# Optimization experiments

Measured on AMD Instinct MI355X. Metric: run time of the kernel, lower is better.

Reference implementation:

```python
import jax, jax.numpy as jnp
import numpy as np

NUM_SUBSET = 3
BN_EPS = 1e-5


def setup_inputs() -> dict:
    key = jax.random.key(0)
    ks = jax.random.split(key, 6)
    N, C, T, V = 32, 192, 256, 25
    x = jax.random.normal(ks[0], (N, C, T, V), dtype=jnp.float32)
    w_in = jax.random.normal(ks[1], (3 * C, C), dtype=jnp.float32) * (1.0 / np.sqrt(C))
    b_in = jax.random.normal(ks[2], (3 * C,), dtype=jnp.float32) * 0.02
    w_ff = jax.random.normal(ks[3], (C, C), dtype=jnp.float32) * (1.0 / np.sqrt(C))
    b_ff = jax.random.normal(ks[4], (C,), dtype=jnp.float32) * 0.02
    bn_gamma = jnp.ones((C,), dtype=jnp.float32)
    bn_beta = jnp.zeros((C,), dtype=jnp.float32)
    bn_mean = jnp.zeros((C,), dtype=jnp.float32)
    bn_var = jnp.ones((C,), dtype=jnp.float32)
    return dict(x=x, w_in=w_in, b_in=b_in, w_ff=w_ff, b_ff=b_ff,
                bn_gamma=bn_gamma, bn_beta=bn_beta, bn_mean=bn_mean, bn_var=bn_var)


def reference(x, w_in, b_in, w_ff, b_ff, bn_gamma, bn_beta, bn_mean, bn_var):
    N, C, T, V = x.shape
    S = NUM_SUBSET
    mid = C // S
    # 1x1 conv QKV projection: (N,C,T,V) x (3C,C) -> (N,3C,T,V)
    qkv = jnp.einsum('nctv,dc->ndtv', x, w_in) + b_in[None, :, None, None]
    qkv = qkv.reshape(N, 3 * S, mid, T, V)
    q, k, v = jnp.split(qkv, 3, axis=1)  # each (N,S,mid,T,V)
    # tanh-normalized attention over time: (N,S,T,T)
    att = jnp.tanh(jnp.einsum('nsctv,nscqv->nstq', q, k) / (mid * V))
    y = jnp.einsum('nstq,nscqv->nsctv', att, v).reshape(N, C, T, V)
    # ff_nett: 1x1 conv + BatchNorm (inference form)
    y = jnp.einsum('nctv,dc->ndtv', y, w_ff) + b_ff[None, :, None, None]
    inv = bn_gamma / jnp.sqrt(bn_var + BN_EPS)
    y = (y - bn_mean[None, :, None, None]) * inv[None, :, None, None] + bn_beta[None, :, None, None]
    # residual + LeakyReLU(0.1)
    z = x + y
    return jnp.where(z >= 0, z, 0.1 * z)
```

## Files before the change

### kernel.cpp

```cpp
#include <hip/hip_runtime.h>

#define TV 6400
#define NCH 192
#define D3 576

typedef unsigned short u16;
typedef unsigned int   u32;

typedef __attribute__((ext_vector_type(8))) short bf16x8;
typedef __attribute__((ext_vector_type(4))) float f32x4;

__device__ __forceinline__ float bf2f(u32 h) { return __uint_as_float(h << 16); }
__device__ __forceinline__ u16 f2bf(float f) {
    u32 u = __float_as_uint(f);
    return (u16)((u + 0x7FFFu + ((u >> 16) & 1u)) >> 16);
}

__global__ __launch_bounds__(256) void k_wcast(const float* __restrict__ w_in,
                                               const float* __restrict__ w_ff,
                                               u32* __restrict__ wb) {
    int i = blockIdx.x * 256 + threadIdx.x;
    float2 f;
    if (i < 55296) f = *(const float2*)(w_in + 2 * i);
    else           f = *(const float2*)(w_ff + 2 * (i - 55296));
    wb[i] = (u32)f2bf(f.x) | ((u32)f2bf(f.y) << 16);
}

__global__ __launch_bounds__(256) void k_trx(const float* __restrict__ x,
                                             u16* __restrict__ x_t) {
    const int p0 = blockIdx.x * 128, c0 = blockIdx.y * 64, n = blockIdx.z;
    const int tid = threadIdx.x;
    __shared__ float L[64][129];
    const float* xn = x + ((size_t)n * NCH + c0) * TV + p0;
#pragma unroll
    for (int r = 0; r < 8; ++r) {
        int idx = tid + 256 * r;
        int c = idx >> 5, p4 = idx & 31;
        float4 v = *(const float4*)(xn + (size_t)c * TV + p4 * 4);
        *(float4*)&L[c][p4 * 4] = v;
    }
    __syncthreads();
    const int row = tid >> 1, ch = (tid & 1) * 32;
    u16* dst = x_t + ((size_t)n * TV + p0 + row) * 192 + c0 + ch;
    u32 buf[16];
#pragma unroll
    for (int j = 0; j < 16; ++j) {
        float f0 = L[ch + 2 * j][row], f1 = L[ch + 2 * j + 1][row];
        buf[j] = (u32)f2bf(f0) | ((u32)f2bf(f1) << 16);
    }
#pragma unroll
    for (int q = 0; q < 4; ++q) {
        uint4 u; u.x = buf[q * 4]; u.y = buf[q * 4 + 1]; u.z = buf[q * 4 + 2]; u.w = buf[q * 4 + 3];
        *(uint4*)(dst + q * 8) = u;
    }
}

__global__ __launch_bounds__(256) void k_qkv(const u16* __restrict__ x_t,
                                             const u16* __restrict__ w_inb,
                                             const float* __restrict__ b_in,
                                             u16* __restrict__ qkv,
                                             u16* __restrict__ qt,
                                             u16* __restrict__ kt) {
    const int p0 = blockIdx.x * 128, n = blockIdx.y;
    const int tid = threadIdx.x;
    const int wid = tid >> 6, lane = tid & 63;
    const int wm = wid & 1, wn = wid >> 1;
    const int ml = lane & 15, kq = lane >> 4;

    __shared__ __align__(16) char Bs[128 * 384];
    __shared__ __align__(16) char As[64 * 384];

#pragma unroll
    for (int r = 0; r < 12; ++r) {
        int idx = tid + 256 * r;
        int row = idx / 24, g = idx - row * 24;
        uint4 v = *(const uint4*)(x_t + ((size_t)n * TV + p0 + row) * 192 + g * 8);
        *(uint4*)(Bs + row * 384 + (((g & ~7) | ((g ^ row) & 7)) << 4)) = v;
    }

    for (int dt = 0; dt < 9; ++dt) {
#pragma unroll
        for (int r = 0; r < 6; ++r) {
            int idx = tid + 256 * r;
            int row = idx / 24, g = idx - row * 24;
            uint4 v = *(const uint4*)(w_inb + (size_t)(dt * 64 + row) * 192 + g * 8);
            *(uint4*)(As + row * 384 + (((g & ~7) | ((g ^ row) & 7)) << 4)) = v;
        }
        __syncthreads();

        f32x4 acc[2][4];
#pragma unroll
        for (int i = 0; i < 2; i++)
#pragma unroll
            for (int j = 0; j < 4; j++)
#pragma unroll
                for (int r = 0; r < 4; r++) acc[i][j][r] = 0.f;

#pragma unroll
        for (int kk = 0; kk < 3; ++kk)
#pragma unroll
            for (int ks = 0; ks < 2; ++ks) {
                int g = kk * 8 + ks * 4 + kq;
                bf16x8 aw[2], bx[4];
#pragma unroll
                for (int mt = 0; mt < 2; ++mt) {
                    int row = wm * 32 + mt * 16 + ml;
                    aw[mt] = *(const bf16x8*)(As + row * 384 + (((g & ~7) | ((g ^ row) & 7)) << 4));
                }
#pragma unroll
                for (int nt = 0; nt < 4; ++nt) {
                    int row = wn * 64 + nt * 16 + ml;
                    bx[nt] = *(const bf16x8*)(Bs + row * 384 + (((g & ~7) | ((g ^ row) & 7)) << 4));
                }
#pragma unroll
                for (int mt = 0; mt < 2; ++mt)
#pragma unroll
                    for (int nt = 0; nt < 4; ++nt)
                        acc[mt][nt] = __builtin_amdgcn_mfma_f32_16x16x32_bf16(aw[mt], bx[nt], acc[mt][nt], 0, 0, 0);
            }

        if (dt < 6) {
            const int s = (dt < 3) ? dt : dt - 3;
            u16* dstb = (dt < 3 ? qt : kt) + ((size_t)(n * 3 + s) * 6400 + p0) * 64;
#pragma unroll
            for (int mt = 0; mt < 2; ++mt) {
                int c = wm * 32 + mt * 16 + kq * 4;
                float4 bias = *(const float4*)(b_in + dt * 64 + c);
#pragma unroll
                for (int nt = 0; nt < 4; ++nt) {
                    int p = wn * 64 + nt * 16 + ml;
                    u32 w0 = (u32)f2bf(acc[mt][nt][0] + bias.x) | ((u32)f2bf(acc[mt][nt][1] + bias.y) << 16);
                    u32 w1 = (u32)f2bf(acc[mt][nt][2] + bias.z) | ((u32)f2bf(acc[mt][nt][3] + bias.w) << 16);
                    uint2 u; u.x = w0; u.y = w1;
                    *(uint2*)(dstb + (size_t)p * 64 + c) = u;
                }
            }
        } else {
#pragma unroll
            for (int mt = 0; mt < 2; ++mt) {
                int d = dt * 64 + wm * 32 + mt * 16 + kq * 4;
                float4 bias = *(const float4*)(b_in + d);
                u16* vdst = qkv + ((size_t)n * D3 + d) * TV;
#pragma unroll
                for (int nt = 0; nt < 4; ++nt) {
                    int p = p0 + wn * 64 + nt * 16 + ml;
                    vdst[(size_t)0 * TV + p] = f2bf(acc[mt][nt][0] + bias.x);
                    vdst[(size_t)1 * TV + p] = f2bf(acc[mt][nt][1] + bias.y);
                    vdst[(size_t)2 * TV + p] = f2bf(acc[mt][nt][2] + bias.z);
                    vdst[(size_t)3 * TV + p] = f2bf(acc[mt][nt][3] + bias.w);
                }
            }
        }
        __syncthreads();
    }
}

__global__ __launch_bounds__(256) void k_scores(const u16* __restrict__ qt,
                                                const u16* __restrict__ kt,
                                                u16* __restrict__ att) {
    const int b = blockIdx.z, t0 = blockIdx.y * 128, q0 = blockIdx.x * 64;
    const int tid = threadIdx.x;
    const int wid = tid >> 6, lane = tid & 63;
    const int wm = wid & 1, wn = wid >> 1;
    const int ml = lane & 15, kq = lane >> 4;

    __shared__ __align__(16) char As[128 * 128];
    __shared__ __align__(16) char Bs[64 * 128];

    f32x4 acc[4][2];
#pragma unroll
    for (int i = 0; i < 4; i++)
#pragma unroll
        for (int j = 0; j < 2; j++)
#pragma unroll
            for (int r = 0; r < 4; r++) acc[i][j][r] = 0.f;

    const u16* qb = qt + (size_t)b * 256 * 1600;
    const u16* kb = kt + (size_t)b * 256 * 1600;

    for (int kc = 0; kc < 1600; kc += 64) {
#pragma unroll
        for (int r = 0; r < 4; r++) {
            int idx = tid + 256 * r;
            int row = idx >> 3, g = idx & 7;
            uint4 v = *(const uint4*)(qb + (size_t)(t0 + row) * 1600 + kc + g * 8);
            *(uint4*)(As + row * 128 + (((g ^ row) & 7) << 4)) = v;
        }
#pragma unroll
        for (int r = 0; r < 2; r++) {
            int idx = tid + 256 * r;
            int row = idx >> 3, g = idx & 7;
            uint4 v = *(const uint4*)(kb + (size_t)(q0 + row) * 1600 + kc + g * 8);
            *(uint4*)(Bs + row * 128 + (((g ^ row) & 7) << 4)) = v;
        }
        __syncthreads();
#pragma unroll
        for (int ks = 0; ks < 2; ks++) {
            int gb = ks * 4 + kq;
            bf16x8 a[4], bb[2];
#pragma unroll
            for (int mt = 0; mt < 4; mt++) {
                int row = wm * 64 + mt * 16 + ml;
                a[mt] = *(const bf16x8*)(As + row * 128 + (((gb ^ row) & 7) << 4));
            }
#pragma unroll
            for (int nt = 0; nt < 2; nt++) {
                int row = wn * 32 + nt * 16 + ml;
                bb[nt] = *(const bf16x8*)(Bs + row * 128 + (((gb ^ row) & 7) << 4));
            }
#pragma unroll
            for (int mt = 0; mt < 4; mt++)
#pragma unroll
                for (int nt = 0; nt < 2; nt++)
                    acc[mt][nt] = __builtin_amdgcn_mfma_f32_16x16x32_bf16(a[mt], bb[nt], acc[mt][nt], 0, 0, 0);
        }
        __syncthreads();
    }

    const float sc = 1.0f / 1600.0f;
    u16* ab = att + (size_t)b * 65536;
#pragma unroll
    for (int mt = 0; mt < 4; mt++)
#pragma unroll
        for (int nt = 0; nt < 2; nt++) {
            int q = q0 + wn * 32 + nt * 16 + ml;
#pragma unroll
            for (int r = 0; r < 4; r++) {
                int t = t0 + wm * 64 + mt * 16 + kq * 4 + r;
                ab[(size_t)t * 256 + q] = f2bf(tanhf(acc[mt][nt][r] * sc));
            }
        }
}

__global__ __launch_bounds__(256) void k_trv(const u16* __restrict__ qkv,
                                             u16* __restrict__ vt) {
    const int q0 = blockIdx.x * 32;
    const int c0 = blockIdx.y * 32;
    const int b  = blockIdx.z;
    const int n = b / 3, s = b % 3;
    const int tid = threadIdx.x;

    __shared__ u16 L[32 * 800];

    const u16* src = qkv + ((size_t)n * D3 + 384 + s * 64 + c0) * TV + q0 * 25;
#pragma unroll
    for (int r = 0; r < 13; ++r) {
        int idx = tid + 256 * r;
        if (idx < 3200) {
            int c = idx / 100, w = idx - 100 * c;
            uint4 v = *(const uint4*)(src + (size_t)c * TV + w * 8);
            *(uint4*)&L[c * 800 + w * 8] = v;
        }
    }
    __syncthreads();

    u16* dst = vt + ((size_t)b * 1600 + c0) * 256 + q0;
#pragma unroll
    for (int r = 0; r < 4; ++r) {
        int idx = tid + 256 * r;
        if (idx < 800) {
            int c = idx / 25, v = idx - 25 * c;
            const u16* lp = &L[c * 800 + v];
            u32 buf[16];
#pragma unroll
            for (int j = 0; j < 16; ++j) {
                u32 lo = lp[(2 * j) * 25];
                u32 hi = lp[(2 * j + 1) * 25];
                buf[j] = lo | (hi << 16);
            }
            u16* dp = dst + (size_t)(v * 64 + c) * 256;
#pragma unroll
            for (int q4 = 0; q4 < 4; ++q4) {
                uint4 u; u.x = buf[q4 * 4]; u.y = buf[q4 * 4 + 1];
                u.z = buf[q4 * 4 + 2]; u.w = buf[q4 * 4 + 3];
                *(uint4*)(dp + q4 * 8) = u;
            }
        }
    }
}

__global__ __launch_bounds__(256) void k_av(const u16* __restrict__ att,
                                            const u16* __restrict__ vt,
                                            u16* __restrict__ y_t) {
    const int b = blockIdx.z, t0 = blockIdx.y * 128, v = blockIdx.x;
    const int n = b / 3, s = b % 3;
    const int tid = threadIdx.x;
    const int wid = tid >> 6, lane = tid & 63;
    const int wm = wid & 1, wn = wid >> 1;
    const int ml = lane & 15, kq = lane >> 4;

    __shared__ __align__(16) char As[128 * 128];
    __shared__ __align__(16) char Bs[64 * 128];

    f32x4 acc[4][2];
#pragma unroll
    for (int i = 0; i < 4; i++)
#pragma unroll
        for (int j = 0; j < 2; j++)
#pragma unroll
            for (int r = 0; r < 4; r++) acc[i][j][r] = 0.f;

    const u16* ab = att + (size_t)b * 65536;
    const u16* vb = vt + ((size_t)b * 1600 + v * 64) * 256;

    for (int kc = 0; kc < 256; kc += 64) {
#pragma unroll
        for (int r = 0; r < 4; r++) {
            int idx = tid + 256 * r;
            int row = idx >> 3, g = idx & 7;
            uint4 u = *(const uint4*)(ab + (size_t)(t0 + row) * 256 + kc + g * 8);
            *(uint4*)(As + row * 128 + (((g ^ row) & 7) << 4)) = u;
        }
#pragma unroll
        for (int r = 0; r < 2; r++) {
            int idx = tid + 256 * r;
            int row = idx >> 3, g = idx & 7;
            uint4 u = *(const uint4*)(vb + (size_t)row * 256 + kc + g * 8);
            *(uint4*)(Bs + row * 128 + (((g ^ row) & 7) << 4)) = u;
        }
        __syncthreads();
#pragma unroll
        for (int ks = 0; ks < 2; ks++) {
            int gb = ks * 4 + kq;
            bf16x8 a[4], bb[2];
#pragma unroll
            for (int mt = 0; mt < 4; mt++) {
                int row = wm * 64 + mt * 16 + ml;
                a[mt] = *(const bf16x8*)(As + row * 128 + (((gb ^ row) & 7) << 4));
            }
#pragma unroll
            for (int nt = 0; nt < 2; nt++) {
                int row = wn * 32 + nt * 16 + ml;
                bb[nt] = *(const bf16x8*)(Bs + row * 128 + (((gb ^ row) & 7) << 4));
            }
#pragma unroll
            for (int mt = 0; mt < 4; mt++)
#pragma unroll
                for (int nt = 0; nt < 2; nt++)
                    acc[mt][nt] = __builtin_amdgcn_mfma_f32_16x16x32_bf16(a[mt], bb[nt], acc[mt][nt], 0, 0, 0);
        }
        __syncthreads();
    }

#pragma unroll
    for (int mt = 0; mt < 4; mt++)
#pragma unroll
        for (int nt = 0; nt < 2; nt++) {
            int cg = s * 64 + wn * 32 + nt * 16 + ml;
#pragma unroll
            for (int r = 0; r < 4; r++) {
                int t = t0 + wm * 64 + mt * 16 + kq * 4 + r;
                y_t[((size_t)n * TV + t * 25 + v) * 192 + cg] = f2bf(acc[mt][nt][r]);
            }
        }
}

__global__ __launch_bounds__(256) void k_ff(const u16* __restrict__ y_t,
                                            const float* __restrict__ x,
                                            const u16* __restrict__ w_ffb,
                                            const float* __restrict__ b_ff,
                                            const float* __restrict__ gamma,
                                            const float* __restrict__ beta,
                                            const float* __restrict__ mean,
                                            const float* __restrict__ var,
                                            float* __restrict__ out) {
    const int n = blockIdx.z, d0 = blockIdx.y * 64, p0 = blockIdx.x * 128;
    const int tid = threadIdx.x;
    const int wid = tid >> 6, lane = tid & 63;
    const int wn = wid;
    const int ml = lane & 15, kq = lane >> 4;

    __shared__ __align__(16) char Aw[64 * 128];
    __shared__ __align__(16) char By[128 * 128];

    f32x4 acc[4][2];
#pragma unroll
    for (int i = 0; i < 4; i++)
#pragma unroll
        for (int j = 0; j < 2; j++)
#pragma unroll
            for (int r = 0; r < 4; r++) acc[i][j][r] = 0.f;

    for (int kc = 0; kc < 192; kc += 64) {
#pragma unroll
        for (int r = 0; r < 2; r++) {
            int idx = tid + 256 * r;
            int row = idx >> 3, g = idx & 7;
            uint4 v = *(const uint4*)(w_ffb + (size_t)(d0 + row) * 192 + kc + g * 8);
            *(uint4*)(Aw + row * 128 + (((g ^ row) & 7) << 4)) = v;
        }
#pragma unroll
        for (int r = 0; r < 4; r++) {
            int idx = tid + 256 * r;
            int row = idx >> 3, g = idx & 7;
            uint4 v = *(const uint4*)(y_t + ((size_t)n * TV + p0 + row) * 192 + kc + g * 8);
            *(uint4*)(By + row * 128 + (((g ^ row) & 7) << 4)) = v;
        }
        __syncthreads();
#pragma unroll
        for (int ks = 0; ks < 2; ks++) {
            int gb = ks * 4 + kq;
            bf16x8 a[4], bb[2];
#pragma unroll
            for (int mt = 0; mt < 4; mt++) {
                int row = mt * 16 + ml;
                a[mt] = *(const bf16x8*)(Aw + row * 128 + (((gb ^ row) & 7) << 4));
            }
#pragma unroll
            for (int nt = 0; nt < 2; nt++) {
                int row = wn * 32 + nt * 16 + ml;
                bb[nt] = *(const bf16x8*)(By + row * 128 + (((gb ^ row) & 7) << 4));
            }
#pragma unroll
            for (int mt = 0; mt < 4; mt++)
#pragma unroll
                for (int nt = 0; nt < 2; nt++)
                    acc[mt][nt] = __builtin_amdgcn_mfma_f32_16x16x32_bf16(a[mt], bb[nt], acc[mt][nt], 0, 0, 0);
        }
        __syncthreads();
    }

#pragma unroll
    for (int mt = 0; mt < 4; mt++)
#pragma unroll
        for (int r = 0; r < 4; r++) {
            int d = d0 + mt * 16 + kq * 4 + r;
            float inv = gamma[d] * rsqrtf(var[d] + 1e-5f);
            float bias = b_ff[d], mu = mean[d], bt = beta[d];
#pragma unroll
            for (int nt = 0; nt < 2; nt++) {
                int p = p0 + wn * 32 + nt * 16 + ml;
                size_t xi = ((size_t)n * NCH + d) * TV + p;
                float v = acc[mt][nt][r] + bias;
                v = (v - mu) * inv + bt;
                float z = x[xi] + v;
                out[xi] = (z >= 0.f) ? z : 0.1f * z;
            }
        }
}

extern "C" void kernel_launch(void* const* d_in, const int* in_sizes, int n_in,
                              void* d_out, int out_size, void* d_ws, size_t ws_size,
                              hipStream_t stream) {
    const float* x     = (const float*)d_in[0];
    const float* w_in  = (const float*)d_in[1];
    const float* b_in  = (const float*)d_in[2];
    const float* w_ff  = (const float*)d_in[3];
    const float* b_ff  = (const float*)d_in[4];
    const float* gamma = (const float*)d_in[5];
    const float* beta  = (const float*)d_in[6];
    const float* mean  = (const float*)d_in[7];
    const float* var   = (const float*)d_in[8];

    u16* qkv = (u16*)d_ws;
    u16* att = (u16*)((char*)d_ws + 235929600ull);
    u16* x_t = (u16*)((char*)d_ws + 248512512ull);
    u16* y_t = x_t;
    u32* wb  = (u32*)((char*)d_ws + 327155712ull);
    u16* w_inb = (u16*)wb;
    u16* w_ffb = w_inb + 110592;
    u16* qt = (u16*)d_out;
    u16* kt = qt + 39321600ull;
    u16* vt = qt;
    float* out = (float*)d_out;

    k_wcast <<<dim3(288),       dim3(256), 0, stream>>>(w_in, w_ff, wb);
    k_trx   <<<dim3(50, 3, 32), dim3(256), 0, stream>>>(x, x_t);
    k_qkv   <<<dim3(50, 32),    dim3(256), 0, stream>>>(x_t, w_inb, b_in, qkv, qt, kt);
    k_scores<<<dim3(4, 2, 96),  dim3(256), 0, stream>>>(qt, kt, att);
    k_trv   <<<dim3(8, 2, 96),  dim3(256), 0, stream>>>(qkv, vt);
    k_av    <<<dim3(25, 2, 96), dim3(256), 0, stream>>>(att, vt, y_t);
    k_ff    <<<dim3(50, 3, 32), dim3(256), 0, stream>>>(y_t, x, w_ffb, b_ff, gamma, beta, mean, var, out);
}
```

Baseline: 637.2 us.

## Fuse x transpose and bf16 cast into QKV projection kernel

Removes the separate k_trx kernel that wrote a transposed bf16 copy of x to workspace. k_qkv now reads fp32 x directly, transposes it through LDS and casts it into the swizzled B tile itself. The position tile is halved to 64, so the grid doubles and each wave computes a 2x2 MFMA tile. This saves one launch and a round trip of x_t through global memory. In exchange, each block reloads the weight tiles for fewer positions and does extra LDS staging.

```diff
diff --git a/kernel.cpp b/kernel.cpp
--- a/kernel.cpp
+++ b/kernel.cpp
@@ -26,56 +26,51 @@
     wb[i] = (u32)f2bf(f.x) | ((u32)f2bf(f.y) << 16);
 }
 
-__global__ __launch_bounds__(256) void k_trx(const float* __restrict__ x,
-                                             u16* __restrict__ x_t) {
-    const int p0 = blockIdx.x * 128, c0 = blockIdx.y * 64, n = blockIdx.z;
-    const int tid = threadIdx.x;
-    __shared__ float L[64][129];
-    const float* xn = x + ((size_t)n * NCH + c0) * TV + p0;
-#pragma unroll
-    for (int r = 0; r < 8; ++r) {
-        int idx = tid + 256 * r;
-        int c = idx >> 5, p4 = idx & 31;
-        float4 v = *(const float4*)(xn + (size_t)c * TV + p4 * 4);
-        *(float4*)&L[c][p4 * 4] = v;
-    }
-    __syncthreads();
-    const int row = tid >> 1, ch = (tid & 1) * 32;
-    u16* dst = x_t + ((size_t)n * TV + p0 + row) * 192 + c0 + ch;
-    u32 buf[16];
-#pragma unroll
-    for (int j = 0; j < 16; ++j) {
-        float f0 = L[ch + 2 * j][row], f1 = L[ch + 2 * j + 1][row];
-        buf[j] = (u32)f2bf(f0) | ((u32)f2bf(f1) << 16);
-    }
-#pragma unroll
-    for (int q = 0; q < 4; ++q) {
-        uint4 u; u.x = buf[q * 4]; u.y = buf[q * 4 + 1]; u.z = buf[q * 4 + 2]; u.w = buf[q * 4 + 3];
-        *(uint4*)(dst + q * 8) = u;
-    }
-}
-
-__global__ __launch_bounds__(256) void k_qkv(const u16* __restrict__ x_t,
+__global__ __launch_bounds__(256) void k_qkv(const float* __restrict__ x,
                                              const u16* __restrict__ w_inb,
                                              const float* __restrict__ b_in,
                                              u16* __restrict__ qkv,
                                              u16* __restrict__ qt,
                                              u16* __restrict__ kt) {
-    const int p0 = blockIdx.x * 128, n = blockIdx.y;
+    const int p0 = blockIdx.x * 64, n = blockIdx.y;
     const int tid = threadIdx.x;
     const int wid = tid >> 6, lane = tid & 63;
-    const int wm = wid & 1, wn = wid >> 1;
+    const int wd = wid & 1, wp = wid >> 1;
     const int ml = lane & 15, kq = lane >> 4;
 
-    __shared__ __align__(16) char Bs[128 * 384];
+    __shared__ __align__(16) char Bs[64 * 384];
     __shared__ __align__(16) char As[64 * 384];
-
-#pragma unroll
-    for (int r = 0; r < 12; ++r) {
-        int idx = tid + 256 * r;
-        int row = idx / 24, g = idx - row * 24;
-        uint4 v = *(const uint4*)(x_t + ((size_t)n * TV + p0 + row) * 192 + g * 8);
-        *(uint4*)(Bs + row * 384 + (((g & ~7) | ((g ^ row) & 7)) << 4)) = v;
+    float* L = (float*)As;
+
+    for (int cc = 0; cc < 3; ++cc) {
+        const float* xn = x + ((size_t)n * NCH + cc * 64) * TV + p0;
+#pragma unroll
+        for (int r = 0; r < 4; ++r) {
+            int idx = tid + 256 * r;
+            int c = idx >> 4, p4 = idx & 15;
+            float4 v = *(const float4*)(xn + (size_t)c * TV + p4 * 4);
+            *(float4*)&L[c * 65 + p4 * 4] = v;
+        }
+        __syncthreads();
+        {
+            int p = tid >> 2, cq = tid & 3;
+            u32 buf[8];
+#pragma unroll
+            for (int j = 0; j < 8; ++j) {
+                float f0 = L[(cq * 16 + 2 * j) * 65 + p];
+                float f1 = L[(cq * 16 + 2 * j + 1) * 65 + p];
+                buf[j] = (u32)f2bf(f0) | ((u32)f2bf(f1) << 16);
+            }
+#pragma unroll
+            for (int h = 0; h < 2; ++h) {
+                int g = cc * 8 + cq * 2 + h;
+                uint4 u;
+                u.x = buf[h * 4]; u.y = buf[h * 4 + 1];
+                u.z = buf[h * 4 + 2]; u.w = buf[h * 4 + 3];
+                *(uint4*)(Bs + p * 384 + (((g & ~7) | ((g ^ p) & 7)) << 4)) = u;
+            }
+        }
+        __syncthreads();
     }
 
     for (int dt = 0; dt < 9; ++dt) {
@@ -88,11 +83,11 @@
         }
         __syncthreads();
 
-        f32x4 acc[2][4];
+        f32x4 acc[2][2];
 #pragma unroll
         for (int i = 0; i < 2; i++)
 #pragma unroll
-            for (int j = 0; j < 4; j++)
+            for (int j = 0; j < 2; j++)
 #pragma unroll
                 for (int r = 0; r < 4; r++) acc[i][j][r] = 0.f;
 
@@ -101,21 +96,21 @@
 #pragma unroll
             for (int ks = 0; ks < 2; ++ks) {
                 int g = kk * 8 + ks * 4 + kq;
-                bf16x8 aw[2], bx[4];
+                bf16x8 aw[2], bx[2];
 #pragma unroll
                 for (int mt = 0; mt < 2; ++mt) {
-                    int row = wm * 32 + mt * 16 + ml;
+                    int row = wd * 32 + mt * 16 + ml;
                     aw[mt] = *(const bf16x8*)(As + row * 384 + (((g & ~7) | ((g ^ row) & 7)) << 4));
                 }
 #pragma unroll
-                for (int nt = 0; nt < 4; ++nt) {
-                    int row = wn * 64 + nt * 16 + ml;
+                for (int nt = 0; nt < 2; ++nt) {
+                    int row = wp * 32 + nt * 16 + ml;
                     bx[nt] = *(const bf16x8*)(Bs + row * 384 + (((g & ~7) | ((g ^ row) & 7)) << 4));
                 }
 #pragma unroll
                 for (int mt = 0; mt < 2; ++mt)
 #pragma unroll
-                    for (int nt = 0; nt < 4; ++nt)
+                    for (int nt = 0; nt < 2; ++nt)
                         acc[mt][nt] = __builtin_amdgcn_mfma_f32_16x16x32_bf16(aw[mt], bx[nt], acc[mt][nt], 0, 0, 0);
             }
 
@@ -124,11 +119,11 @@
             u16* dstb = (dt < 3 ? qt : kt) + ((size_t)(n * 3 + s) * 6400 + p0) * 64;
 #pragma unroll
             for (int mt = 0; mt < 2; ++mt) {
-                int c = wm * 32 + mt * 16 + kq * 4;
+                int c = wd * 32 + mt * 16 + kq * 4;
                 float4 bias = *(const float4*)(b_in + dt * 64 + c);
 #pragma unroll
-                for (int nt = 0; nt < 4; ++nt) {
-                    int p = wn * 64 + nt * 16 + ml;
+                for (int nt = 0; nt < 2; ++nt) {
+                    int p = wp * 32 + nt * 16 + ml;
                     u32 w0 = (u32)f2bf(acc[mt][nt][0] + bias.x) | ((u32)f2bf(acc[mt][nt][1] + bias.y) << 16);
                     u32 w1 = (u32)f2bf(acc[mt][nt][2] + bias.z) | ((u32)f2bf(acc[mt][nt][3] + bias.w) << 16);
                     uint2 u; u.x = w0; u.y = w1;
@@ -138,12 +133,12 @@
         } else {
 #pragma unroll
             for (int mt = 0; mt < 2; ++mt) {
-                int d = dt * 64 + wm * 32 + mt * 16 + kq * 4;
+                int d = dt * 64 + wd * 32 + mt * 16 + kq * 4;
                 float4 bias = *(const float4*)(b_in + d);
                 u16* vdst = qkv + ((size_t)n * D3 + d) * TV;
 #pragma unroll
-                for (int nt = 0; nt < 4; ++nt) {
-                    int p = p0 + wn * 64 + nt * 16 + ml;
+                for (int nt = 0; nt < 2; ++nt) {
+                    int p = p0 + wp * 32 + nt * 16 + ml;
                     vdst[(size_t)0 * TV + p] = f2bf(acc[mt][nt][0] + bias.x);
                     vdst[(size_t)1 * TV + p] = f2bf(acc[mt][nt][1] + bias.y);
                     vdst[(size_t)2 * TV + p] = f2bf(acc[mt][nt][2] + bias.z);
@@ -454,8 +449,7 @@
 
     u16* qkv = (u16*)d_ws;
     u16* att = (u16*)((char*)d_ws + 235929600ull);
-    u16* x_t = (u16*)((char*)d_ws + 248512512ull);
-    u16* y_t = x_t;
+    u16* y_t = (u16*)((char*)d_ws + 248512512ull);
     u32* wb  = (u32*)((char*)d_ws + 327155712ull);
     u16* w_inb = (u16*)wb;
     u16* w_ffb = w_inb + 110592;
@@ -464,11 +458,10 @@
     u16* vt = qt;
     float* out = (float*)d_out;
 
-    k_wcast <<<dim3(288),       dim3(256), 0, stream>>>(w_in, w_ff, wb);
-    k_trx   <<<dim3(50, 3, 32), dim3(256), 0, stream>>>(x, x_t);
-    k_qkv   <<<dim3(50, 32),    dim3(256), 0, stream>>>(x_t, w_inb, b_in, qkv, qt, kt);
-    k_scores<<<dim3(4, 2, 96),  dim3(256), 0, stream>>>(qt, kt, att);
-    k_trv   <<<dim3(8, 2, 96),  dim3(256), 0, stream>>>(qkv, vt);
-    k_av    <<<dim3(25, 2, 96), dim3(256), 0, stream>>>(att, vt, y_t);
-    k_ff    <<<dim3(50, 3, 32), dim3(256), 0, stream>>>(y_t, x, w_ffb, b_ff, gamma, beta, mean, var, out);
-}
+    k_wcast <<<dim3(288),        dim3(256), 0, stream>>>(w_in, w_ff, wb);
+    k_qkv   <<<dim3(100, 32),    dim3(256), 0, stream>>>(x, w_inb, b_in, qkv, qt, kt);
+    k_scores<<<dim3(4, 2, 96),   dim3(256), 0, stream>>>(qt, kt, att);
+    k_trv   <<<dim3(8, 2, 96),   dim3(256), 0, stream>>>(qkv, vt);
+    k_av    <<<dim3(25, 2, 96),  dim3(256), 0, stream>>>(att, vt, y_t);
+    k_ff    <<<dim3(50, 3, 32),  dim3(256), 0, stream>>>(y_t, x, w_ffb, b_ff, gamma, beta, mean, var, out);
+}
```

After: 598.5 us. 6.1% less time.

## Fuse x transpose into QKV GEMM and pre-swizzle weights into MFMA fragment order

Applied to the files above, without the earlier changes.

Removes the separate k_trx kernel. k_qkv now reads fp32 x directly, converts it to bf16 and writes it into the swizzled LDS tile. The weight cast kernel writes w_in in per-lane MFMA fragment order, so k_qkv loads A operands straight from global memory. This drops the per-dt LDS staging of weights and the two barriers per iteration. In exchange, the x loads are strided 4-byte reads with partial coalescing, and weight fragments are re-read from L2 by every block.

```diff
diff --git a/kernel.cpp b/kernel.cpp
--- a/kernel.cpp
+++ b/kernel.cpp
@@ -21,42 +21,25 @@
                                                u32* __restrict__ wb) {
     int i = blockIdx.x * 256 + threadIdx.x;
     float2 f;
-    if (i < 55296) f = *(const float2*)(w_in + 2 * i);
-    else           f = *(const float2*)(w_ff + 2 * (i - 55296));
+    if (i < 55296) {
+        int frag = i >> 8, r = i & 255;
+        int lane = r >> 2, ep = r & 3;
+        int ks = frag & 1;
+        int t1 = frag >> 1;
+        int kk = t1 % 3;
+        int t2 = t1 / 3;
+        int mt = t2 & 1, wd = (t2 >> 1) & 1, dt = t2 >> 2;
+        int d = dt * 64 + wd * 32 + mt * 16 + (lane & 15);
+        int c = (kk * 8 + ks * 4 + (lane >> 4)) * 8 + ep * 2;
+        f = *(const float2*)(w_in + d * 192 + c);
+    } else {
+        f = *(const float2*)(w_ff + 2 * (i - 55296));
+    }
     wb[i] = (u32)f2bf(f.x) | ((u32)f2bf(f.y) << 16);
 }
 
-__global__ __launch_bounds__(256) void k_trx(const float* __restrict__ x,
-                                             u16* __restrict__ x_t) {
-    const int p0 = blockIdx.x * 128, c0 = blockIdx.y * 64, n = blockIdx.z;
-    const int tid = threadIdx.x;
-    __shared__ float L[64][129];
-    const float* xn = x + ((size_t)n * NCH + c0) * TV + p0;
-#pragma unroll
-    for (int r = 0; r < 8; ++r) {
-        int idx = tid + 256 * r;
-        int c = idx >> 5, p4 = idx & 31;
-        float4 v = *(const float4*)(xn + (size_t)c * TV + p4 * 4);
-        *(float4*)&L[c][p4 * 4] = v;
-    }
-    __syncthreads();
-    const int row = tid >> 1, ch = (tid & 1) * 32;
-    u16* dst = x_t + ((size_t)n * TV + p0 + row) * 192 + c0 + ch;
-    u32 buf[16];
-#pragma unroll
-    for (int j = 0; j < 16; ++j) {
-        float f0 = L[ch + 2 * j][row], f1 = L[ch + 2 * j + 1][row];
-        buf[j] = (u32)f2bf(f0) | ((u32)f2bf(f1) << 16);
-    }
-#pragma unroll
-    for (int q = 0; q < 4; ++q) {
-        uint4 u; u.x = buf[q * 4]; u.y = buf[q * 4 + 1]; u.z = buf[q * 4 + 2]; u.w = buf[q * 4 + 3];
-        *(uint4*)(dst + q * 8) = u;
-    }
-}
-
-__global__ __launch_bounds__(256) void k_qkv(const u16* __restrict__ x_t,
-                                             const u16* __restrict__ w_inb,
+__global__ __launch_bounds__(256) void k_qkv(const float* __restrict__ x,
+                                             const u16* __restrict__ w_frag,
                                              const float* __restrict__ b_in,
                                              u16* __restrict__ qkv,
                                              u16* __restrict__ qt,
@@ -68,26 +51,27 @@
     const int ml = lane & 15, kq = lane >> 4;
 
     __shared__ __align__(16) char Bs[128 * 384];
-    __shared__ __align__(16) char As[64 * 384];
-
-#pragma unroll
-    for (int r = 0; r < 12; ++r) {
-        int idx = tid + 256 * r;
-        int row = idx / 24, g = idx - row * 24;
-        uint4 v = *(const uint4*)(x_t + ((size_t)n * TV + p0 + row) * 192 + g * 8);
-        *(uint4*)(Bs + row * 384 + (((g & ~7) | ((g ^ row) & 7)) << 4)) = v;
-    }
+
+    {
+        const int p = tid >> 1, ch = tid & 1;
+        const float* xp = x + (size_t)n * NCH * TV + p0 + p;
+#pragma unroll
+        for (int j = 0; j < 12; ++j) {
+            int g = ch * 12 + j;
+            u32 buf[4];
+#pragma unroll
+            for (int e = 0; e < 4; ++e) {
+                float f0 = xp[(size_t)(g * 8 + 2 * e) * TV];
+                float f1 = xp[(size_t)(g * 8 + 2 * e + 1) * TV];
+                buf[e] = (u32)f2bf(f0) | ((u32)f2bf(f1) << 16);
+            }
+            uint4 u; u.x = buf[0]; u.y = buf[1]; u.z = buf[2]; u.w = buf[3];
+            *(uint4*)(Bs + p * 384 + (((g & ~7) | ((g ^ p) & 7)) << 4)) = u;
+        }
+    }
+    __syncthreads();
 
     for (int dt = 0; dt < 9; ++dt) {
-#pragma unroll
-        for (int r = 0; r < 6; ++r) {
-            int idx = tid + 256 * r;
-            int row = idx / 24, g = idx - row * 24;
-            uint4 v = *(const uint4*)(w_inb + (size_t)(dt * 64 + row) * 192 + g * 8);
-            *(uint4*)(As + row * 384 + (((g & ~7) | ((g ^ row) & 7)) << 4)) = v;
-        }
-        __syncthreads();
-
         f32x4 acc[2][4];
 #pragma unroll
         for (int i = 0; i < 2; i++)
@@ -104,8 +88,8 @@
                 bf16x8 aw[2], bx[4];
 #pragma unroll
                 for (int mt = 0; mt < 2; ++mt) {
-                    int row = wm * 32 + mt * 16 + ml;
-                    aw[mt] = *(const bf16x8*)(As + row * 384 + (((g & ~7) | ((g ^ row) & 7)) << 4));
+                    int frag = ((((dt * 2 + wm) * 2 + mt) * 3 + kk) * 2 + ks);
+                    aw[mt] = *(const bf16x8*)(w_frag + (size_t)frag * 512 + lane * 8);
                 }
 #pragma unroll
                 for (int nt = 0; nt < 4; ++nt) {
@@ -151,7 +135,6 @@
                 }
             }
         }
-        __syncthreads();
     }
 }
 
@@ -454,21 +437,19 @@
 
     u16* qkv = (u16*)d_ws;
     u16* att = (u16*)((char*)d_ws + 235929600ull);
-    u16* x_t = (u16*)((char*)d_ws + 248512512ull);
-    u16* y_t = x_t;
+    u16* y_t = (u16*)((char*)d_ws + 248512512ull);
     u32* wb  = (u32*)((char*)d_ws + 327155712ull);
-    u16* w_inb = (u16*)wb;
-    u16* w_ffb = w_inb + 110592;
+    u16* w_frag = (u16*)wb;
+    u16* w_ffb  = w_frag + 110592;
     u16* qt = (u16*)d_out;
     u16* kt = qt + 39321600ull;
     u16* vt = qt;
     float* out = (float*)d_out;
 
-    k_wcast <<<dim3(288),       dim3(256), 0, stream>>>(w_in, w_ff, wb);
-    k_trx   <<<dim3(50, 3, 32), dim3(256), 0, stream>>>(x, x_t);
-    k_qkv   <<<dim3(50, 32),    dim3(256), 0, stream>>>(x_t, w_inb, b_in, qkv, qt, kt);
-    k_scores<<<dim3(4, 2, 96),  dim3(256), 0, stream>>>(qt, kt, att);
-    k_trv   <<<dim3(8, 2, 96),  dim3(256), 0, stream>>>(qkv, vt);
-    k_av    <<<dim3(25, 2, 96), dim3(256), 0, stream>>>(att, vt, y_t);
-    k_ff    <<<dim3(50, 3, 32), dim3(256), 0, stream>>>(y_t, x, w_ffb, b_ff, gamma, beta, mean, var, out);
-}
+    k_wcast <<<dim3(288),        dim3(256), 0, stream>>>(w_in, w_ff, wb);
+    k_qkv   <<<dim3(50, 32),     dim3(256), 0, stream>>>(x, w_frag, b_in, qkv, qt, kt);
+    k_scores<<<dim3(4, 2, 96),   dim3(256), 0, stream>>>(qt, kt, att);
+    k_trv   <<<dim3(8, 2, 96),   dim3(256), 0, stream>>>(qkv, vt);
+    k_av    <<<dim3(25, 2, 96),  dim3(256), 0, stream>>>(att, vt, y_t);
+    k_ff    <<<dim3(50, 3, 32),  dim3(256), 0, stream>>>(y_t, x, w_ffb, b_ff, gamma, beta, mean, var, out);
+}
```

After: 616.3 us. 1.03x faster.
